# Optimization experiments

Hardware: AMD Instinct MI355X
Metric: run time of the kernel (lower is better)

Reference implementation:

```python
import math
import jax, jax.numpy as jnp
import numpy as np

HEADS = 8
D_MODEL = 256


def positional_encoding_2d(c, h, w):
    # faithful port of wzlxjtu/PositionalEncoding2D
    d = c // 2
    div_term = jnp.exp(jnp.arange(0.0, d, 2, dtype=jnp.float32) * (-(math.log(10000.0) / d)))  # [d//2? no: d/2 entries -> d//2]
    pos_w = jnp.arange(0.0, w, dtype=jnp.float32)[:, None] * div_term  # [w, d//2]
    pos_h = jnp.arange(0.0, h, dtype=jnp.float32)[:, None] * div_term  # [h, d//2]
    pe = jnp.zeros((c, h, w), dtype=jnp.float32)
    sw = jnp.broadcast_to(jnp.sin(pos_w).T[:, None, :], (div_term.shape[0], h, w))
    cw = jnp.broadcast_to(jnp.cos(pos_w).T[:, None, :], (div_term.shape[0], h, w))
    sh = jnp.broadcast_to(jnp.sin(pos_h).T[:, :, None], (div_term.shape[0], h, w))
    ch = jnp.broadcast_to(jnp.cos(pos_h).T[:, :, None], (div_term.shape[0], h, w))
    pe = pe.at[0:d:2].set(sw)
    pe = pe.at[1:d:2].set(cw)
    pe = pe.at[d::2].set(sh)
    pe = pe.at[d + 1::2].set(ch)
    return pe


def setup_inputs() -> dict:
    key = jax.random.key(0)
    ks = jax.random.split(key, 9)
    b, c, h, w = 2, D_MODEL, 64, 64
    x = jax.random.normal(ks[0], (b, c, h, w), dtype=jnp.float32)
    s = 0.02
    Wq = jax.random.normal(ks[1], (c, c), dtype=jnp.float32) * s
    Wk = jax.random.normal(ks[2], (c, c), dtype=jnp.float32) * s
    Wv = jax.random.normal(ks[3], (c, c), dtype=jnp.float32) * s
    Wo = jax.random.normal(ks[4], (c, c), dtype=jnp.float32) * s
    bq = jax.random.normal(ks[5], (c,), dtype=jnp.float32) * s
    bk = jax.random.normal(ks[6], (c,), dtype=jnp.float32) * s
    bv = jax.random.normal(ks[7], (c,), dtype=jnp.float32) * s
    bo = jax.random.normal(ks[8], (c,), dtype=jnp.float32) * s
    return {"x": x, "Wq": Wq, "bq": bq, "Wk": Wk, "bk": bk,
            "Wv": Wv, "bv": bv, "Wo": Wo, "bo": bo}


def reference(x, Wq, bq, Wk, bk, Wv, bv, Wo, bo):
    b, c, h, w = x.shape
    dk = c // HEADS
    pe = positional_encoding_2d(c, h, w)
    x2 = x + pe[None]                                   # [b,c,h,w]
    tok = x2.reshape(b, c, h * w).transpose(0, 2, 1)    # [b,N,c]
    q = (tok @ Wq.T + bq).reshape(b, -1, HEADS, dk).transpose(0, 2, 1, 3)  # [b,H,N,dk]
    k = (tok @ Wk.T + bk).reshape(b, -1, HEADS, dk).transpose(0, 2, 1, 3)
    v = (tok @ Wv.T + bv).reshape(b, -1, HEADS, dk).transpose(0, 2, 1, 3)
    scores = jnp.einsum('bhnd,bhmd->bhnm', q, k) / math.sqrt(dk)  # [b,H,N,N]
    attn = jax.nn.softmax(scores, axis=-1)
    out = jnp.einsum('bhnm,bhmd->bhnd', attn, v)        # [b,H,N,dk]
    concat = out.transpose(0, 2, 1, 3).reshape(b, -1, c)  # [b,N,c]
    proj = concat @ Wo.T + bo                           # [b,N,c]
    return proj.transpose(0, 2, 1).reshape(b, c, h, w)
```

## Files before the change

kernel.cpp:

```cpp
#include <hip/hip_runtime.h>
#include <hip/hip_bf16.h>
#include <cstdint>

typedef float f32x4 __attribute__((ext_vector_type(4)));
typedef __bf16 bf16x8 __attribute__((ext_vector_type(8)));
typedef __bf16 bf16x4 __attribute__((ext_vector_type(4)));
typedef __bf16 bf16x2 __attribute__((ext_vector_type(2)));
typedef short short4v __attribute__((ext_vector_type(4)));
typedef uint32_t uint2v __attribute__((ext_vector_type(2)));

#define MFMA_K32(A, B, C) __builtin_amdgcn_mfma_f32_16x16x32_bf16((A), (B), (C), 0, 0, 0)

#if __has_builtin(__builtin_amdgcn_mfma_f32_16x16x16bf16_1k)
#define MFMA_K16(A, B, C) __builtin_amdgcn_mfma_f32_16x16x16bf16_1k((A), (B), (C), 0, 0, 0)
#elif __has_builtin(__builtin_amdgcn_mfma_f32_16x16x16_bf16)
static __device__ __forceinline__ f32x4 mfma_k16_alt(short4v a, short4v b, f32x4 c) {
    return __builtin_amdgcn_mfma_f32_16x16x16_bf16(*(bf16x4*)&a, *(bf16x4*)&b, c, 0, 0, 0);
}
#define MFMA_K16(A, B, C) mfma_k16_alt((A), (B), (C))
#else
#define MFMA_K16(A, B, C) (C)
#endif

#if __has_builtin(__builtin_amdgcn_exp2f)
#define EXP2(x) __builtin_amdgcn_exp2f(x)
#else
#define EXP2(x) exp2f(x)
#endif

static __device__ __forceinline__ uint16_t f2b(float f) {
    uint32_t u = __float_as_uint(f);
    uint32_t r = (u + 0x7fffu + ((u >> 16) & 1u)) >> 16;
    return (uint16_t)r;
}

static __device__ __forceinline__ uint32_t packbf(float a, float b) {
#if __has_builtin(__builtin_amdgcn_cvt_pk_bf16_f32)
    bf16x2 v = __builtin_amdgcn_cvt_pk_bf16_f32(a, b);
    return *(uint32_t*)&v;
#else
    uint32_t ua = __float_as_uint(a);
    ua += 0x7fffu + ((ua >> 16) & 1u);
    uint32_t ub = __float_as_uint(b);
    ub += 0x7fffu + ((ub >> 16) & 1u);
    return __builtin_amdgcn_perm(ub, ua, 0x07060302);
#endif
}

__global__ __launch_bounds__(256) void wconv_pe(const float* __restrict__ wq,
                                                const float* __restrict__ wk,
                                                const float* __restrict__ wv,
                                                const float* __restrict__ wo,
                                                uint16_t* __restrict__ dst,
                                                float* __restrict__ pet) {
    int bid = blockIdx.x, t = threadIdx.x;
    if (bid < 1024) {
        int idx = bid * 256 + t;
        int which = idx >> 16, off = idx & 65535;
        const float* s = (which == 0) ? wq : (which == 1) ? wk : (which == 2) ? wv : wo;
        dst[idx] = f2b(s[off]);
    } else {
        int idx = (bid - 1024) * 256 + t;
        int cc = idx >> 6, p = idx & 63;
        int i = (cc & 127) >> 1;
        float dt = __expf((float)(2 * i) * -0.07195578415606394f);
        float sv, cv;
        __sincosf((float)p * dt, &sv, &cv);
        pet[idx] = (cc & 1) ? cv : sv;
    }
}

__global__ __launch_bounds__(256) void peadd(const float* __restrict__ x,
                                             const float* __restrict__ pet,
                                             uint16_t* __restrict__ tok) {
    __shared__ uint16_t T[64][65];
    int t = threadIdx.x, bid = blockIdx.x;
    int nt = bid & 63, ct = (bid >> 6) & 3, bb = bid >> 8;
    int n0 = nt << 6, c0 = ct << 6;
    int nl = t & 63, cq = t >> 6;
    int n = n0 + nl;
    int posh = n0 >> 6;
#pragma unroll
    for (int p = 0; p < 16; ++p) {
        int cl = cq * 16 + p;
        int cc = c0 + cl;
        float pe = pet[cc * 64 + ((cc & 128) ? posh : nl)];
        T[cl][nl] = f2b(x[((size_t)(bb * 256 + cc) << 12) + n] + pe);
    }
    __syncthreads();
#pragma unroll
    for (int p = 0; p < 16; ++p) {
        int tl = cq * 16 + p;
        tok[(((size_t)(bb << 12) | (n0 + tl)) << 8) + c0 + nl] = T[nl][tl];
    }
}

__global__ __launch_bounds__(256) void qkv_gemm(const uint16_t* __restrict__ tok,
                                                const uint16_t* __restrict__ Wall,
                                                const float* __restrict__ bq,
                                                const float* __restrict__ bk,
                                                const float* __restrict__ bv,
                                                uint16_t* __restrict__ qo,
                                                uint16_t* __restrict__ ko,
                                                uint16_t* __restrict__ vo) {
    __shared__ __align__(16) uint16_t WS[64][264];
    int tid = threadIdx.x, wv = tid >> 6, lane = tid & 63;
    int c16 = lane & 15, quad = lane >> 4;
    int M0 = blockIdx.x * 64 + wv * 16;
    int O0 = blockIdx.y * 64;
    const uint16_t* arow = tok + (size_t)(M0 + c16) * 256;
    bf16x8 af[8];
#pragma unroll
    for (int kk = 0; kk < 8; ++kk) af[kk] = *(const bf16x8*)(arow + kk * 32 + quad * 8);
    f32x4 zero = {0.f, 0.f, 0.f, 0.f};
    int bb = M0 >> 12, n = (M0 + c16) & 4095;
    int srow = tid >> 5, sch = (tid & 31) << 3;
    for (int mat = 0; mat < 3; ++mat) {
        const uint16_t* Wg = Wall + (size_t)mat * 65536 + (size_t)O0 * 256;
        __syncthreads();
#pragma unroll
        for (int p = 0; p < 8; ++p)
            *(bf16x8*)(&WS[p * 8 + srow][sch]) = *(const bf16x8*)(Wg + (p * 8 + srow) * 256 + sch);
        __syncthreads();
        f32x4 acc[4] = {zero, zero, zero, zero};
#pragma unroll
        for (int kk = 0; kk < 8; ++kk) {
            int k0 = kk * 32 + quad * 8;
#pragma unroll
            for (int nb = 0; nb < 4; ++nb)
                acc[nb] = MFMA_K32(*(const bf16x8*)(&WS[nb * 16 + c16][k0]),
                                   af[kk], acc[nb]);
        }
        const float* bias = (mat == 0) ? bq : (mat == 1) ? bk : bv;
        if (mat < 2) {
            float scale = (mat == 0) ? 0.25505654134660127f : 1.0f;
            uint16_t* dst = (mat == 0) ? qo : ko;
#pragma unroll
            for (int nb = 0; nb < 4; ++nb) {
                int o = O0 + nb * 16 + quad * 4;
                f32x4 bi = *(const f32x4*)(bias + o);
                int h = o >> 5, dd = o & 31;
                uint2v pk;
                pk[0] = packbf((acc[nb][0] + bi[0]) * scale, (acc[nb][1] + bi[1]) * scale);
                pk[1] = packbf((acc[nb][2] + bi[2]) * scale, (acc[nb][3] + bi[3]) * scale);
                *(uint2v*)(dst + ((size_t)(bb * 8 + h) * 4096 + n) * 32 + dd) = pk;
            }
        } else {
#pragma unroll
            for (int nb = 0; nb < 4; ++nb)
#pragma unroll
                for (int r = 0; r < 4; ++r) {
                    int o = O0 + nb * 16 + quad * 4 + r;
                    vo[((size_t)(bb * 8 + (o >> 5)) * 32 + (o & 31)) * 4096 + n] =
                        f2b(acc[nb][r] + bias[o]);
                }
        }
    }
}

static __device__ __forceinline__ void attn_qblock(const bf16x8 (&kf)[4],
                                                   const short4v (&vf)[2][4],
                                                   bf16x8 qf, f32x4& oA, f32x4& oB,
                                                   f32x4& oS) {
    f32x4 zero = {0.f, 0.f, 0.f, 0.f};
    const short4v ones = {0x3F80, 0x3F80, 0x3F80, 0x3F80};
    f32x4 s[4];
#pragma unroll
    for (int kc = 0; kc < 4; ++kc) s[kc] = MFMA_K32(kf[kc], qf, zero);
#pragma unroll
    for (int kc = 0; kc < 4; ++kc) {
#pragma unroll
        for (int r = 0; r < 4; ++r) s[kc][r] = EXP2(s[kc][r]);
        union { short4v s4; uint32_t u[2]; } pa;
        pa.u[0] = packbf(s[kc][0], s[kc][1]);
        pa.u[1] = packbf(s[kc][2], s[kc][3]);
        oA = MFMA_K16(pa.s4, vf[0][kc], oA);
        oB = MFMA_K16(pa.s4, vf[1][kc], oB);
        oS = MFMA_K16(pa.s4, ones, oS);
    }
}

__global__ __launch_bounds__(512, 4) void flash(const uint16_t* __restrict__ qb,
                                                const uint16_t* __restrict__ kb,
                                                const uint16_t* __restrict__ vtb,
                                                uint16_t* __restrict__ concat) {
    __shared__ __align__(16) char smem[38912];
    int tid = threadIdx.x, wv = tid >> 6, lane = tid & 63;
    int c16 = lane & 15, quad = lane >> 4;
    int half = tid >> 8, t2 = tid & 255;
    int bh = blockIdx.y;
    int q0 = (blockIdx.x << 7) + (wv & 3) * 32;
    size_t base = (size_t)bh << 12;

    uint16_t* KT = (uint16_t*)(smem + half * 19456);
    uint16_t* VT = (uint16_t*)(smem + half * 19456 + 10240);

    const uint16_t* kgp = kb + (base + (size_t)half * 2048 + (t2 >> 2)) * 32 + (t2 & 3) * 8;
    const uint16_t* vgp = vtb + ((size_t)bh * 32 + (t2 >> 3)) * 4096 + half * 2048 + (t2 & 7) * 8;
    uint16_t* kls = KT + (t2 >> 2) * 40 + (t2 & 3) * 8;
    uint16_t* vls = VT + (t2 >> 3) * 72 + (t2 & 7) * 8;

    bf16x8 qf0 = *(const bf16x8*)(qb + (base + q0 + c16) * 32 + quad * 8);
    bf16x8 qf1 = *(const bf16x8*)(qb + (base + q0 + 16 + c16) * 32 + quad * 8);

    f32x4 zero = {0.f, 0.f, 0.f, 0.f};
    f32x4 o00 = zero, o01 = zero, o10 = zero, o11 = zero;
    f32x4 oS0 = zero, oS1 = zero;

    {
        bf16x8 kr = *(const bf16x8*)kgp;
        bf16x8 vr = *(const bf16x8*)vgp;
        *(bf16x8*)kls = kr;
        *(bf16x8*)vls = vr;
    }
    __syncthreads();

    for (int kt = 0; kt < 32; ++kt) {
        int cur = kt & 1;
        int kn = (kt + 1) & 31;
        bf16x8 kr = *(const bf16x8*)(kgp + (size_t)kn * 2048);
        bf16x8 vr = *(const bf16x8*)(vgp + kn * 64);
        const uint16_t* kfp = KT + cur * 2560 + c16 * 40 + quad * 8;
        const uint16_t* vfp = VT + cur * 2304 + c16 * 72 + quad * 4;
        bf16x8 kf[4];
        short4v vf[2][4];
#pragma unroll
        for (int kc = 0; kc < 4; ++kc) kf[kc] = *(const bf16x8*)(kfp + kc * 640);
#pragma unroll
        for (int kc = 0; kc < 4; ++kc) {
            vf[0][kc] = *(const short4v*)(vfp + kc * 16);
            vf[1][kc] = *(const short4v*)(vfp + 1152 + kc * 16);
        }
        attn_qblock(kf, vf, qf0, o00, o01, oS0);
        attn_qblock(kf, vf, qf1, o10, o11, oS1);
        *(bf16x8*)(kls + (cur ^ 1) * 2560) = kr;
        *(bf16x8*)(vls + (cur ^ 1) * 2304) = vr;
        __syncthreads();
    }

    float* ov = (float*)smem;
    if (wv >= 4) {
        float* d = ov + ((wv - 4) * 64 + lane) * 25;
#pragma unroll
        for (int r = 0; r < 4; ++r) {
            d[r] = o00[r]; d[4 + r] = o01[r]; d[8 + r] = o10[r]; d[12 + r] = o11[r];
            d[16 + r] = oS0[r]; d[20 + r] = oS1[r];
        }
    }
    __syncthreads();
    if (wv < 4) {
        const float* s = ov + (wv * 64 + lane) * 25;
#pragma unroll
        for (int r = 0; r < 4; ++r) {
            o00[r] += s[r]; o01[r] += s[4 + r]; o10[r] += s[8 + r]; o11[r] += s[12 + r];
            oS0[r] += s[16 + r]; oS1[r] += s[20 + r];
        }
        int h = bh & 7, bb = bh >> 3;
#pragma unroll
        for (int r = 0; r < 4; ++r) {
            float i0 = 1.f / oS0[r];
            float i1 = 1.f / oS1[r];
            int n = q0 + quad * 4 + r;
            size_t row0 = ((size_t)bb * 4096 + n) * 256 + h * 32;
            size_t row1 = ((size_t)bb * 4096 + n + 16) * 256 + h * 32;
            concat[row0 + c16]      = f2b(o00[r] * i0);
            concat[row0 + 16 + c16] = f2b(o01[r] * i0);
            concat[row1 + c16]      = f2b(o10[r] * i1);
            concat[row1 + 16 + c16] = f2b(o11[r] * i1);
        }
    }
}

__global__ __launch_bounds__(256) void proj_gemm(const uint16_t* __restrict__ concat,
                                                 const uint16_t* __restrict__ Wo,
                                                 const float* __restrict__ bo,
                                                 float* __restrict__ out) {
    __shared__ __align__(16) uint16_t WS[64][264];
    int tid = threadIdx.x, wv = tid >> 6, lane = tid & 63;
    int c16 = lane & 15, quad = lane >> 4;
    int M0 = blockIdx.x * 64 + wv * 16;
    int O0 = blockIdx.y * 64;
    int srow = tid >> 5, sch = (tid & 31) << 3;
    const uint16_t* Wg = Wo + (size_t)O0 * 256;
#pragma unroll
    for (int p = 0; p < 8; ++p)
        *(bf16x8*)(&WS[p * 8 + srow][sch]) = *(const bf16x8*)(Wg + (p * 8 + srow) * 256 + sch);
    const uint16_t* crow = concat + (size_t)(M0 + c16) * 256;
    bf16x8 af[8];
#pragma unroll
    for (int kk = 0; kk < 8; ++kk) af[kk] = *(const bf16x8*)(crow + kk * 32 + quad * 8);
    __syncthreads();
    f32x4 zero = {0.f, 0.f, 0.f, 0.f};
    f32x4 acc[4] = {zero, zero, zero, zero};
#pragma unroll
    for (int kk = 0; kk < 8; ++kk) {
        int k0 = kk * 32 + quad * 8;
#pragma unroll
        for (int nb = 0; nb < 4; ++nb)
            acc[nb] = MFMA_K32(*(const bf16x8*)(&WS[nb * 16 + c16][k0]),
                               af[kk], acc[nb]);
    }
    int bb = M0 >> 12, n = (M0 + c16) & 4095;
#pragma unroll
    for (int nb = 0; nb < 4; ++nb)
#pragma unroll
        for (int r = 0; r < 4; ++r) {
            int o = O0 + nb * 16 + quad * 4 + r;
            out[((size_t)(bb * 256 + o) << 12) + n] = acc[nb][r] + bo[o];
        }
}

extern "C" void kernel_launch(void* const* d_in, const int* in_sizes, int n_in,
                              void* d_out, int out_size, void* d_ws, size_t ws_size,
                              hipStream_t stream) {
    const float* x  = (const float*)d_in[0];
    const float* Wq = (const float*)d_in[1];
    const float* bq = (const float*)d_in[2];
    const float* Wk = (const float*)d_in[3];
    const float* bk = (const float*)d_in[4];
    const float* Wv = (const float*)d_in[5];
    const float* bv = (const float*)d_in[6];
    const float* Wo = (const float*)d_in[7];
    const float* bo = (const float*)d_in[8];
    float* out = (float*)d_out;

    uint16_t* ws   = (uint16_t*)d_ws;
    uint16_t* Wb   = ws;
    uint16_t* tok  = Wb + 4 * 65536;
    uint16_t* q    = tok + 2097152;
    uint16_t* k    = q + 2097152;
    uint16_t* vt   = k + 2097152;
    uint16_t* cc   = vt + 2097152;
    float*    pet  = (float*)(cc + 2097152);

    wconv_pe<<<1088, 256, 0, stream>>>(Wq, Wk, Wv, Wo, Wb, pet);
    peadd<<<512, 256, 0, stream>>>(x, pet, tok);
    qkv_gemm<<<dim3(128, 4), 256, 0, stream>>>(tok, Wb, bq, bk, bv, q, k, vt);
    flash<<<dim3(32, 16), 512, 0, stream>>>(q, k, vt, cc);
    proj_gemm<<<dim3(128, 4), 256, 0, stream>>>(cc, Wb + 3 * 65536, bo, out);
}
```

Before: 149.6 us.

## Fuse weight conversion and PE into consumers; stage QKV outputs through LDS

Removes the separate weight-conversion and positional-encoding kernel. Weights are now converted from fp32 to bf16 on the fly inside each GEMM block, and the PE sin/cos is computed inline in peadd. The QKV epilogue also stages results in a shared-memory tile, so Q, K and transposed V can be written with coalesced 16-byte stores instead of scattered 8-byte and 2-byte stores. This drops one launch and an intermediate buffer round-trip. The cost is more fp32 weight traffic per block, redundant conversions across blocks, extra transcendental math in peadd, and additional barriers.

```diff
diff --git a/kernel.cpp b/kernel.cpp
--- a/kernel.cpp
+++ b/kernel.cpp
@@ -47,31 +47,7 @@
 #endif
 }
 
-__global__ __launch_bounds__(256) void wconv_pe(const float* __restrict__ wq,
-                                                const float* __restrict__ wk,
-                                                const float* __restrict__ wv,
-                                                const float* __restrict__ wo,
-                                                uint16_t* __restrict__ dst,
-                                                float* __restrict__ pet) {
-    int bid = blockIdx.x, t = threadIdx.x;
-    if (bid < 1024) {
-        int idx = bid * 256 + t;
-        int which = idx >> 16, off = idx & 65535;
-        const float* s = (which == 0) ? wq : (which == 1) ? wk : (which == 2) ? wv : wo;
-        dst[idx] = f2b(s[off]);
-    } else {
-        int idx = (bid - 1024) * 256 + t;
-        int cc = idx >> 6, p = idx & 63;
-        int i = (cc & 127) >> 1;
-        float dt = __expf((float)(2 * i) * -0.07195578415606394f);
-        float sv, cv;
-        __sincosf((float)p * dt, &sv, &cv);
-        pet[idx] = (cc & 1) ? cv : sv;
-    }
-}
-
 __global__ __launch_bounds__(256) void peadd(const float* __restrict__ x,
-                                             const float* __restrict__ pet,
                                              uint16_t* __restrict__ tok) {
     __shared__ uint16_t T[64][65];
     int t = threadIdx.x, bid = blockIdx.x;
@@ -79,12 +55,17 @@
     int n0 = nt << 6, c0 = ct << 6;
     int nl = t & 63, cq = t >> 6;
     int n = n0 + nl;
-    int posh = n0 >> 6;
+    float posh = (float)nt;
+    float posw = (float)nl;
 #pragma unroll
     for (int p = 0; p < 16; ++p) {
         int cl = cq * 16 + p;
         int cc = c0 + cl;
-        float pe = pet[cc * 64 + ((cc & 128) ? posh : nl)];
+        int i = (cc & 127) >> 1;
+        float dt = __expf((float)(2 * i) * -0.07195578415606394f);
+        float sv, cv;
+        __sincosf(((cc & 128) ? posh : posw) * dt, &sv, &cv);
+        float pe = (cc & 1) ? cv : sv;
         T[cl][nl] = f2b(x[((size_t)(bb * 256 + cc) << 12) + n] + pe);
     }
     __syncthreads();
@@ -96,7 +77,9 @@
 }
 
 __global__ __launch_bounds__(256) void qkv_gemm(const uint16_t* __restrict__ tok,
-                                                const uint16_t* __restrict__ Wall,
+                                                const float* __restrict__ wqf,
+                                                const float* __restrict__ wkf,
+                                                const float* __restrict__ wvf,
                                                 const float* __restrict__ bq,
                                                 const float* __restrict__ bk,
                                                 const float* __restrict__ bv,
@@ -104,23 +87,32 @@
                                                 uint16_t* __restrict__ ko,
                                                 uint16_t* __restrict__ vo) {
     __shared__ __align__(16) uint16_t WS[64][264];
-    int tid = threadIdx.x, wv = tid >> 6, lane = tid & 63;
+    __shared__ __align__(16) uint16_t VS[64][72];
+    int tid = threadIdx.x, wvi = tid >> 6, lane = tid & 63;
     int c16 = lane & 15, quad = lane >> 4;
-    int M0 = blockIdx.x * 64 + wv * 16;
+    int Mblk = blockIdx.x * 64;
+    int M0 = Mblk + wvi * 16;
     int O0 = blockIdx.y * 64;
     const uint16_t* arow = tok + (size_t)(M0 + c16) * 256;
     bf16x8 af[8];
 #pragma unroll
     for (int kk = 0; kk < 8; ++kk) af[kk] = *(const bf16x8*)(arow + kk * 32 + quad * 8);
     f32x4 zero = {0.f, 0.f, 0.f, 0.f};
-    int bb = M0 >> 12, n = (M0 + c16) & 4095;
-    int srow = tid >> 5, sch = (tid & 31) << 3;
+    int bb = Mblk >> 12;
+    int nloc = Mblk & 4095;
+    int rt = tid >> 2, seg = tid & 3;
     for (int mat = 0; mat < 3; ++mat) {
-        const uint16_t* Wg = Wall + (size_t)mat * 65536 + (size_t)O0 * 256;
+        const float* Wg = ((mat == 0) ? wqf : (mat == 1) ? wkf : wvf) + (size_t)O0 * 256;
         __syncthreads();
 #pragma unroll
-        for (int p = 0; p < 8; ++p)
-            *(bf16x8*)(&WS[p * 8 + srow][sch]) = *(const bf16x8*)(Wg + (p * 8 + srow) * 256 + sch);
+        for (int p = 0; p < 16; ++p) {
+            int idx = p * 1024 + tid * 4;
+            f32x4 w4 = *(const f32x4*)(Wg + idx);
+            uint2v pk;
+            pk[0] = packbf(w4[0], w4[1]);
+            pk[1] = packbf(w4[2], w4[3]);
+            *(uint2v*)(&WS[idx >> 8][idx & 255]) = pk;
+        }
         __syncthreads();
         f32x4 acc[4] = {zero, zero, zero, zero};
 #pragma unroll
@@ -131,29 +123,39 @@
                 acc[nb] = MFMA_K32(*(const bf16x8*)(&WS[nb * 16 + c16][k0]),
                                    af[kk], acc[nb]);
         }
-        const float* bias = (mat == 0) ? bq : (mat == 1) ? bk : bv;
         if (mat < 2) {
+            const float* bias = (mat == 0) ? bq : bk;
             float scale = (mat == 0) ? 0.25505654134660127f : 1.0f;
-            uint16_t* dst = (mat == 0) ? qo : ko;
 #pragma unroll
             for (int nb = 0; nb < 4; ++nb) {
                 int o = O0 + nb * 16 + quad * 4;
                 f32x4 bi = *(const f32x4*)(bias + o);
-                int h = o >> 5, dd = o & 31;
                 uint2v pk;
                 pk[0] = packbf((acc[nb][0] + bi[0]) * scale, (acc[nb][1] + bi[1]) * scale);
                 pk[1] = packbf((acc[nb][2] + bi[2]) * scale, (acc[nb][3] + bi[3]) * scale);
-                *(uint2v*)(dst + ((size_t)(bb * 8 + h) * 4096 + n) * 32 + dd) = pk;
+                *(uint2v*)(&VS[wvi * 16 + c16][nb * 16 + quad * 4]) = pk;
             }
+            __syncthreads();
+            uint16_t* dst = (mat == 0) ? qo : ko;
+            int o0 = O0 + seg * 16;
+            int h = o0 >> 5, d0 = o0 & 31;
+            size_t addr = ((size_t)(bb * 8 + h) * 4096 + nloc + rt) * 32 + d0;
+            *(bf16x8*)(dst + addr) = *(const bf16x8*)(&VS[rt][seg * 16]);
+            *(bf16x8*)(dst + addr + 8) = *(const bf16x8*)(&VS[rt][seg * 16 + 8]);
         } else {
+            const float* bias = bv;
 #pragma unroll
             for (int nb = 0; nb < 4; ++nb)
 #pragma unroll
                 for (int r = 0; r < 4; ++r) {
                     int o = O0 + nb * 16 + quad * 4 + r;
-                    vo[((size_t)(bb * 8 + (o >> 5)) * 32 + (o & 31)) * 4096 + n] =
-                        f2b(acc[nb][r] + bias[o]);
+                    VS[nb * 16 + quad * 4 + r][wvi * 16 + c16] = f2b(acc[nb][r] + bias[o]);
                 }
+            __syncthreads();
+            int o = O0 + rt;
+            size_t addr = ((size_t)(bb * 8 + (o >> 5)) * 32 + (o & 31)) * 4096 + nloc + seg * 16;
+            *(bf16x8*)(vo + addr) = *(const bf16x8*)(&VS[rt][seg * 16]);
+            *(bf16x8*)(vo + addr + 8) = *(const bf16x8*)(&VS[rt][seg * 16 + 8]);
         }
     }
 }
@@ -272,19 +274,24 @@
 }
 
 __global__ __launch_bounds__(256) void proj_gemm(const uint16_t* __restrict__ concat,
-                                                 const uint16_t* __restrict__ Wo,
+                                                 const float* __restrict__ wof,
                                                  const float* __restrict__ bo,
                                                  float* __restrict__ out) {
     __shared__ __align__(16) uint16_t WS[64][264];
-    int tid = threadIdx.x, wv = tid >> 6, lane = tid & 63;
+    int tid = threadIdx.x, wvi = tid >> 6, lane = tid & 63;
     int c16 = lane & 15, quad = lane >> 4;
-    int M0 = blockIdx.x * 64 + wv * 16;
+    int M0 = blockIdx.x * 64 + wvi * 16;
     int O0 = blockIdx.y * 64;
-    int srow = tid >> 5, sch = (tid & 31) << 3;
-    const uint16_t* Wg = Wo + (size_t)O0 * 256;
-#pragma unroll
-    for (int p = 0; p < 8; ++p)
-        *(bf16x8*)(&WS[p * 8 + srow][sch]) = *(const bf16x8*)(Wg + (p * 8 + srow) * 256 + sch);
+    const float* Wg = wof + (size_t)O0 * 256;
+#pragma unroll
+    for (int p = 0; p < 16; ++p) {
+        int idx = p * 1024 + tid * 4;
+        f32x4 w4 = *(const f32x4*)(Wg + idx);
+        uint2v pk;
+        pk[0] = packbf(w4[0], w4[1]);
+        pk[1] = packbf(w4[2], w4[3]);
+        *(uint2v*)(&WS[idx >> 8][idx & 255]) = pk;
+    }
     const uint16_t* crow = concat + (size_t)(M0 + c16) * 256;
     bf16x8 af[8];
 #pragma unroll
@@ -325,17 +332,14 @@
     float* out = (float*)d_out;
 
     uint16_t* ws   = (uint16_t*)d_ws;
-    uint16_t* Wb   = ws;
-    uint16_t* tok  = Wb + 4 * 65536;
+    uint16_t* tok  = ws;
     uint16_t* q    = tok + 2097152;
     uint16_t* k    = q + 2097152;
     uint16_t* vt   = k + 2097152;
     uint16_t* cc   = vt + 2097152;
-    float*    pet  = (float*)(cc + 2097152);
-
-    wconv_pe<<<1088, 256, 0, stream>>>(Wq, Wk, Wv, Wo, Wb, pet);
-    peadd<<<512, 256, 0, stream>>>(x, pet, tok);
-    qkv_gemm<<<dim3(128, 4), 256, 0, stream>>>(tok, Wb, bq, bk, bv, q, k, vt);
+
+    peadd<<<512, 256, 0, stream>>>(x, tok);
+    qkv_gemm<<<dim3(128, 4), 256, 0, stream>>>(tok, Wq, Wk, Wv, bq, bk, bv, q, k, vt);
     flash<<<dim3(32, 16), 512, 0, stream>>>(q, k, vt, cc);
-    proj_gemm<<<dim3(128, 4), 256, 0, stream>>>(cc, Wb + 3 * 65536, bo, out);
-}
+    proj_gemm<<<dim3(128, 4), 256, 0, stream>>>(cc, Wo, bo, out);
+}
```

Measured after the change: 153.2 us. 2.4% more time.
